# Kernel optimization log

Hardware: AMD Instinct MI355X
Metric: run time of the kernel (lower is better)

## Reference

```python
import jax, jax.numpy as jnp
import numpy as np

EPS = 1e-6
K = 20                 # k-NN neighbors (init default)
NEG_SLOPE_CONV = 0.2   # VNLinearLeakyReLU negative_slope in conv_pos / actvn_c
NEG_SLOPE_BLOCK = 0.0  # VNResnetBlockFC uses VNLeakyReLU(negative_slope=0.0)


def vn_linear(w, x):
    # w: [O, C], x: [B, C, 3, ...] -> [B, O, 3, ...]
    return jnp.einsum('oc,bc...->bo...', w, x)


def vn_leaky(x, d, slope):
    # Vector-neuron leaky ReLU: project onto learned direction d per channel.
    dot = jnp.sum(x * d, axis=2, keepdims=True)          # sum over 3-vector dim
    dsq = jnp.sum(d * d, axis=2, keepdims=True)
    x_neg = x - (dot / (dsq + EPS)) * d
    return slope * x + (1.0 - slope) * jnp.where(dot >= 0, x, x_neg)


def vn_lin_leaky(wf, wd, x, slope):
    return vn_leaky(vn_linear(wf, x), vn_linear(wd, x), slope)


def knn_idx(pts, k):
    # pts: [B, N, 3]; largest of negative squared distance = nearest (incl. self)
    d2 = jnp.sum(pts * pts, axis=-1)
    score = 2.0 * jnp.einsum('bnd,bmd->bnm', pts, pts) - d2[:, :, None] - d2[:, None, :]
    _, idx = jax.lax.top_k(score, k)
    return idx                                           # [B, N, k]


def graph_feature_cross(p, k):
    # p: [B, N, 3] -> edge features [B, 3(ch: rel, center, cross), 3(vec), N, k]
    idx = knn_idx(p, k)
    nb = jax.vmap(lambda pts, ix: pts[ix])(p, idx)       # [B, N, k, 3] gather
    ctr = jnp.broadcast_to(p[:, :, None, :], nb.shape)
    cross = jnp.cross(nb, ctr)
    feat = jnp.stack([nb - ctr, ctr, cross], axis=3)     # [B, N, k, 3ch, 3vec]
    return jnp.transpose(feat, (0, 3, 4, 1, 2))


def vn_resnet_block(x, wd0, wf0, wd1, wf1, wsc):
    net = vn_linear(wf0, vn_leaky(x, vn_linear(wd0, x), NEG_SLOPE_BLOCK))
    dx = vn_linear(wf1, vn_leaky(net, vn_linear(wd1, net), NEG_SLOPE_BLOCK))
    return vn_linear(wsc, x) + dx


def setup_inputs() -> dict:
    key = jax.random.key(0)
    ks = jax.random.split(key, 11)
    B, N = 4, 2048
    c_dim, hd = 128, 128
    s = lambda k_, sh, fan: (jax.random.normal(k_, sh, jnp.float32) / np.sqrt(fan).astype(np.float32))
    return {
        'p': jax.random.normal(ks[0], (B, N, 3), jnp.float32),
        'w_conv_feat': s(ks[1], (128, 3), 3),
        'w_conv_dir': s(ks[2], (128, 3), 3),
        'w_fc_pos': s(ks[3], (2 * hd, 128), 128),
        'blk_dir0': s(ks[4], (5, 2 * hd, 2 * hd), 2 * hd),
        'blk_fc0': s(ks[5], (5, hd, 2 * hd), 2 * hd),
        'blk_dir1': s(ks[6], (5, hd, hd), hd),
        'blk_fc1': s(ks[7], (5, hd, hd), hd),
        'blk_sc': s(ks[8], (5, hd, 2 * hd), 2 * hd),
        'w_actc_dir': s(ks[9], (hd, hd), hd),
        'w_fc_c': s(ks[10], (c_dim, hd), hd),
    }


def reference(p, w_conv_feat, w_conv_dir, w_fc_pos, blk_dir0, blk_fc0,
              blk_dir1, blk_fc1, blk_sc, w_actc_dir, w_fc_c):
    feat = graph_feature_cross(p, K)                     # [B, 3, 3, N, K]
    net = vn_lin_leaky(w_conv_feat, w_conv_dir, feat, NEG_SLOPE_CONV)
    net = net.mean(axis=-1)                              # pool over k -> [B,128,3,N]
    net = vn_linear(w_fc_pos, net)                       # [B,256,3,N]
    net = vn_resnet_block(net, blk_dir0[0], blk_fc0[0], blk_dir1[0], blk_fc1[0], blk_sc[0])
    for i in range(1, 5):                                # fixed 5-block stack
        pooled = jnp.broadcast_to(net.mean(axis=-1, keepdims=True), net.shape)
        net = jnp.concatenate([net, pooled], axis=1)     # [B,256,3,N]
        net = vn_resnet_block(net, blk_dir0[i], blk_fc0[i], blk_dir1[i], blk_fc1[i], blk_sc[i])
    net = net.mean(axis=-1)                              # global pool -> [B,128,3]
    net = vn_leaky(net, vn_linear(w_actc_dir, net), NEG_SLOPE_CONV)
    return vn_linear(w_fc_c, net)                        # c: [B,128,3]
```

## Files before the change

### kernel.cpp

```cpp
#include <hip/hip_runtime.h>
#include <math.h>

#define NPT 2048
#define BB 4
#define KNN 20
#define EPSV 1e-6f

typedef unsigned short u16;
typedef unsigned int u32;
typedef _Float16 half8 __attribute__((ext_vector_type(8)));
typedef __attribute__((ext_vector_type(4))) float f32x4;
typedef __attribute__((ext_vector_type(4))) u32 uint4v;

#define MFMAH(a,b,c) __builtin_amdgcn_mfma_f32_16x16x32_f16((a),(b),(c),0,0,0)

__device__ __forceinline__ u16 f2h(float f) {
    _Float16 h = (_Float16)f;
    return __builtin_bit_cast(u16, h);
}
__device__ __forceinline__ float h2f(u16 b) {
    return (float)__builtin_bit_cast(_Float16, b);
}

__global__ __launch_bounds__(256)
void knn_edge_kernel(const float* __restrict__ p,
                     const float* __restrict__ wf, const float* __restrict__ wd,
                     u16* __restrict__ net1) {
    int bn = blockIdx.x;
    int b = bn >> 11, n = bn & (NPT - 1);
    const float* pb = p + (size_t)b * NPT * 3;
    float qx = pb[n*3+0], qy = pb[n*3+1], qz = pb[n*3+2];
    float qq = qx*qx + qy*qy + qz*qz;
    __shared__ u32 keys[NPT];
    __shared__ int hist[4][256];
    __shared__ int wtot[4];
    __shared__ int sh_byte, sh_ngt, sure_cnt, tie_cnt;
    __shared__ int tie_m[64];
    __shared__ int sel[KNN];
    __shared__ float nb[KNN][3];
    int tid = threadIdx.x;
    int lane = tid & 63, wv = tid >> 6;
    for (int m = tid; m < NPT; m += 256) {
        float px = pb[m*3+0], py = pb[m*3+1], pz = pb[m*3+2];
        float sc = 2.f*(qx*px + qy*py + qz*pz) - qq - (px*px + py*py + pz*pz);
        u32 u = __builtin_bit_cast(u32, sc);
        keys[m] = u ^ (u32)(((int)u >> 31) | (int)0x80000000);
    }
    if (tid == 0) { sure_cnt = 0; tie_cnt = 0; }
    __syncthreads();
    u32 prefix = 0; int need = KNN;
    for (int pass = 3; pass >= 0; --pass) {
        int shift = pass * 8;
        u32 maskhi = (pass == 3) ? 0u : (0xFFFFFFFFu << (shift + 8));
        hist[0][tid] = 0; hist[1][tid] = 0; hist[2][tid] = 0; hist[3][tid] = 0;
        __syncthreads();
        int prevbin = -1, cnt = 0;
        #pragma unroll
        for (int j = 0; j < 8; ++j) {
            u32 key = keys[tid + 256*j];
            int bin = ((key & maskhi) == (prefix & maskhi)) ? (int)((key >> shift) & 255) : -1;
            if (bin == prevbin) { ++cnt; }
            else {
                if (prevbin >= 0) atomicAdd(&hist[wv][prevbin], cnt);
                prevbin = bin; cnt = 1;
            }
        }
        if (prevbin >= 0) atomicAdd(&hist[wv][prevbin], cnt);
        __syncthreads();
        int own = hist[0][tid] + hist[1][tid] + hist[2][tid] + hist[3][tid];
        int sum = own;
        #pragma unroll
        for (int off = 1; off < 64; off <<= 1) {
            int v = __shfl_down(sum, off, 64);
            if (lane + off < 64) sum += v;
        }
        if (lane == 0) wtot[wv] = sum;
        __syncthreads();
        int addhi = 0;
        #pragma unroll
        for (int w2 = 0; w2 < 4; ++w2) if (w2 > wv) addhi += wtot[w2];
        int cnt_ge = sum + addhi;
        int cnt_gt = cnt_ge - own;
        if (cnt_ge >= need && cnt_gt < need) { sh_byte = tid; sh_ngt = cnt_gt; }
        __syncthreads();
        prefix |= ((u32)sh_byte) << shift;
        need -= sh_ngt;
        __syncthreads();
    }
    u32 T = prefix;
    #pragma unroll
    for (int j = 0; j < 8; ++j) {
        int m = tid + 256*j;
        u32 key = keys[m];
        if (key > T) {
            int slot = atomicAdd(&sure_cnt, 1);
            sel[slot] = m;
        } else if (key == T) {
            int t = atomicAdd(&tie_cnt, 1);
            if (t < 64) tie_m[t] = m;
        }
    }
    __syncthreads();
    if (tid == 0) {
        int base = sure_cnt;
        int r = KNN - base;
        int tc = tie_cnt;
        if (tc == r) {
            for (int t2 = 0; t2 < r; ++t2) sel[base + t2] = tie_m[t2];
        } else if (tc <= 64) {
            for (int t2 = 0; t2 < r; ++t2) {
                int best = 1 << 30, bj = 0;
                for (int t3 = 0; t3 < tc; ++t3)
                    if (tie_m[t3] < best) { best = tie_m[t3]; bj = t3; }
                tie_m[bj] = 1 << 30;
                sel[base + t2] = best;
            }
        } else {
            int got = 0;
            for (int m = 0; m < NPT && got < r; ++m)
                if (keys[m] == T) { sel[base + got] = m; ++got; }
        }
    }
    __syncthreads();
    if (tid < KNN) {
        int j = sel[tid];
        nb[tid][0] = pb[j*3+0]; nb[tid][1] = pb[j*3+1]; nb[tid][2] = pb[j*3+2];
    }
    __syncthreads();
    {
        float* part = (float*)keys;
        int o = tid & 127, kh = tid >> 7;
        float wfa = wf[o*3+0], wfb = wf[o*3+1], wfc = wf[o*3+2];
        float wda = wd[o*3+0], wdb = wd[o*3+1], wdc = wd[o*3+2];
        float cx = qx, cy = qy, cz = qz;
        float a0 = 0.f, a1 = 0.f, a2 = 0.f;
        int k0 = kh * 10;
        #pragma unroll
        for (int k = 0; k < 10; ++k) {
            float nx = nb[k0+k][0], ny = nb[k0+k][1], nz = nb[k0+k][2];
            float rx = nx-cx, ry = ny-cy, rz = nz-cz;
            float sx = ny*cz - nz*cy;
            float sy = nz*cx - nx*cz;
            float sz = nx*cy - ny*cx;
            float fx = wfa*rx + wfb*cx + wfc*sx;
            float fy = wfa*ry + wfb*cy + wfc*sy;
            float fz = wfa*rz + wfb*cz + wfc*sz;
            float dx0 = wda*rx + wdb*cx + wdc*sx;
            float dy0 = wda*ry + wdb*cy + wdc*sy;
            float dz0 = wda*rz + wdb*cz + wdc*sz;
            float dot = fx*dx0 + fy*dy0 + fz*dz0;
            float dsq = dx0*dx0 + dy0*dy0 + dz0*dz0;
            float t = dot / (dsq + EPSV);
            bool pos = dot >= 0.f;
            float gx = pos ? fx : (fx - t*dx0);
            float gy = pos ? fy : (fy - t*dy0);
            float gz = pos ? fz : (fz - t*dz0);
            a0 += 0.2f*fx + 0.8f*gx;
            a1 += 0.2f*fy + 0.8f*gy;
            a2 += 0.2f*fz + 0.8f*gz;
        }
        if (kh == 1) { part[o*3+0] = a0; part[o*3+1] = a1; part[o*3+2] = a2; }
        __syncthreads();
        if (kh == 0) {
            a0 += part[o*3+0]; a1 += part[o*3+1]; a2 += part[o*3+2];
            const float s = 1.f / (float)KNN;
            net1[(size_t)(b*6144 +          n)*128 + o] = f2h(a0*s);
            net1[(size_t)(b*6144 + 2048  + n)*128 + o] = f2h(a1*s);
            net1[(size_t)(b*6144 + 4096  + n)*128 + o] = f2h(a2*s);
        }
    }
}

template<int O, int C1, int C2, bool POOL, bool BIASED>
__global__ __launch_bounds__(256) void gemm_plain(
    const u16* __restrict__ W1, int ldw1,
    const u16* __restrict__ X1, int sx1,
    const u16* __restrict__ W2, int ldw2,
    const u16* __restrict__ X2, int sx2,
    const float* __restrict__ WscF, const float* __restrict__ PmPrev,
    u16* __restrict__ Y, int sy,
    float* __restrict__ PmOut)
{
    __shared__ __align__(16) char smem[64*132*4];
    __shared__ float pms[128];
    __shared__ float biasS_s[128];
    const int m0 = blockIdx.x * 64;
    const int ob = blockIdx.y * 128;
    const int b   = m0 / 6144;
    const int vec = (m0 % 6144) / 2048;
    const int tid = threadIdx.x;
    const int lane = tid & 63;
    const int wid = __builtin_amdgcn_readfirstlane(tid >> 6);
    const int wr = wid & 1, wc = wid >> 1;
    const int l15 = lane & 15, l4 = lane >> 4;

    if (BIASED) {
        if (tid < 128) pms[tid] = PmPrev[(size_t)(b*128 + tid)*3 + vec];
        __syncthreads();
        if (tid < 128) {
            const float* wrow = WscF + (size_t)tid*256 + 128;
            float s = 0.f;
            #pragma unroll 4
            for (int c = 0; c < 128; ++c) s += wrow[c]*pms[c];
            biasS_s[tid] = s;
        }
        __syncthreads();
    }

    f32x4 acc[4][2];
    #pragma unroll
    for (int io = 0; io < 4; ++io) {
        float bv[4];
        #pragma unroll
        for (int r = 0; r < 4; ++r)
            bv[r] = BIASED ? biasS_s[wr*64 + io*16 + l4*4 + r] : 0.f;
        #pragma unroll
        for (int jc = 0; jc < 2; ++jc)
            #pragma unroll
            for (int r = 0; r < 4; ++r) acc[io][jc][r] = bv[r];
    }

    constexpr int NS = (C1 + C2) / 64;
    auto ldaddr = [&](int st, int u) -> const u16* {
        const bool ph2 = (st >= C1/64);
        const u16* w = ph2 ? W2 : W1; const u16* x = ph2 ? X2 : X1;
        int ldw = ph2 ? ldw2 : ldw1; int sx = ph2 ? sx2 : sx1;
        int cc = (ph2 ? (st - C1/64) : st) * 64;
        if (u < 1024) {
            int row = u >> 3, q = u & 7;
            return w + (size_t)(ob + row)*ldw + cc + q*8;
        }
        int uu = u - 1024;
        int row = uu >> 3, q = uu & 7;
        return x + (size_t)(m0 + row)*sx + cc + q*8;
    };
    auto lds_dst = [&](int u) -> char* {
        if (u < 1024) { int row = u >> 3, q = u & 7; return smem + row*144 + q*16; }
        int uu = u - 1024;
        int row = uu >> 3, q = uu & 7;
        return smem + 18432 + row*144 + q*16;
    };

    uint4v pf[6];
    #pragma unroll
    for (int j = 0; j < 6; ++j) pf[j] = *reinterpret_cast<const uint4v*>(ldaddr(0, tid + 256*j));
    #pragma unroll
    for (int j = 0; j < 6; ++j) *reinterpret_cast<uint4v*>(lds_dst(tid + 256*j)) = pf[j];

    for (int st = 0; st < NS; ++st) {
        __syncthreads();
        if (st + 1 < NS) {
            #pragma unroll
            for (int j = 0; j < 6; ++j)
                pf[j] = *reinterpret_cast<const uint4v*>(ldaddr(st+1, tid + 256*j));
        }
        #pragma unroll
        for (int ks = 0; ks < 2; ++ks) {
            half8 fA[4], fB[2];
            #pragma unroll
            for (int io = 0; io < 4; ++io)
                fA[io] = *reinterpret_cast<const half8*>(smem + (wr*64 + io*16 + l15)*144 + ks*64 + l4*16);
            #pragma unroll
            for (int i = 0; i < 2; ++i)
                fB[i] = *reinterpret_cast<const half8*>(smem + 18432 + (wc*32 + i*16 + l15)*144 + ks*64 + l4*16);
            #pragma unroll
            for (int io = 0; io < 4; ++io)
                #pragma unroll
                for (int jc = 0; jc < 2; ++jc)
                    acc[io][jc] = MFMAH(fA[io], fB[jc], acc[io][jc]);
        }
        __syncthreads();
        if (st + 1 < NS) {
            #pragma unroll
            for (int j = 0; j < 6; ++j)
                *reinterpret_cast<uint4v*>(lds_dst(tid + 256*j)) = pf[j];
        }
    }

    float* sd = (float*)smem;
    #pragma unroll
    for (int io = 0; io < 4; ++io)
        #pragma unroll
        for (int jc = 0; jc < 2; ++jc) {
            int jj = wc*32 + jc*16 + l15;
            int orow = wr*64 + io*16 + l4*4;
            *reinterpret_cast<f32x4*>(sd + jj*132 + orow) = acc[io][jc];
        }
    __syncthreads();

    #pragma unroll
    for (int rep = 0; rep < 4; ++rep) {
        int task = tid + 256*rep;
        int oc = task & 15, ml = task >> 4;
        const float* dp = sd + ml*132 + oc*8;
        u32 hw[4];
        #pragma unroll
        for (int e2 = 0; e2 < 4; ++e2)
            hw[e2] = (u32)f2h(dp[2*e2]) | ((u32)f2h(dp[2*e2+1]) << 16);
        *reinterpret_cast<uint4v*>(Y + (size_t)(m0 + ml)*sy + ob + oc*8) =
            (uint4v){hw[0],hw[1],hw[2],hw[3]};
    }

    if (POOL) {
        int o_l = tid & 127, half = tid >> 7;
        float sum = 0.f;
        #pragma unroll 8
        for (int c = 0; c < 32; ++c) sum += sd[(half*32 + c)*132 + o_l];
        atomicAdd(&PmOut[(size_t)(b*128 + o_l)*3 + vec], sum * (1.f/(float)NPT));
    }
}

template<int O, int CIN, bool VIRT>
__global__ __launch_bounds__(256) void gemm_dir(
    const u16* __restrict__ W_, int ldw,
    const u16* __restrict__ X1, int sx,
    const float* __restrict__ WdF, const float* __restrict__ Pm,
    u16* __restrict__ Ov, int so,
    float* __restrict__ PmZero)
{
    __shared__ __align__(16) char smem[96*132*4];
    __shared__ float pmd[384];
    __shared__ float biasD_s[384];
    const int gx = blockIdx.x;
    const int b  = gx >> 6;
    const int n0 = (gx & 63) * 32;
    const int ob = blockIdx.y * 128;
    const int tid = threadIdx.x;
    const int lane = tid & 63;
    const int wid = __builtin_amdgcn_readfirstlane(tid >> 6);
    const int wr = wid & 1, wc = wid >> 1;
    const int l15 = lane & 15, l4 = lane >> 4;

    if (PmZero != nullptr && gx == 0 && blockIdx.y == 0)
        for (int t = tid; t < 1536; t += 256) PmZero[t] = 0.f;

    if (VIRT) {
        for (int t = tid; t < 384; t += 256) pmd[t] = Pm[(size_t)b*384 + t];
        __syncthreads();
        for (int t = tid; t < 384; t += 256) {
            int o_l = t / 3, v = t - o_l*3;
            const float* wrow = WdF + (size_t)(ob + o_l)*256 + 128;
            float s = 0.f;
            #pragma unroll 4
            for (int c = 0; c < 128; ++c) s += wrow[c]*pmd[c*3 + v];
            biasD_s[t] = s;
        }
        __syncthreads();
    }

    f32x4 acc[4][3];
    #pragma unroll
    for (int io = 0; io < 4; ++io)
        #pragma unroll
        for (int jc = 0; jc < 3; ++jc) {
            int v = (wc*48 + jc*16) >> 5;
            #pragma unroll
            for (int r = 0; r < 4; ++r) {
                int o_l = wr*64 + io*16 + l4*4 + r;
                acc[io][jc][r] = VIRT ? biasD_s[o_l*3 + v] : 0.f;
            }
        }

    constexpr int NS = CIN / 64;
    auto ldaddr = [&](int st, int u) -> const u16* {
        int cc = st*64;
        if (u < 1024) {
            int row = u >> 3, q = u & 7;
            return W_ + (size_t)(ob + row)*ldw + cc + q*8;
        }
        int uu = u - 1024;
        int row = uu >> 3, q = uu & 7;
        int m = b*6144 + (row >> 5)*2048 + n0 + (row & 31);
        return X1 + (size_t)m*sx + cc + q*8;
    };
    auto lds_dst = [&](int u) -> char* {
        if (u < 1024) { int row = u >> 3, q = u & 7; return smem + row*144 + q*16; }
        int uu = u - 1024;
        int row = uu >> 3, q = uu & 7;
        return smem + 18432 + row*144 + q*16;
    };

    uint4v pf[7];
    #pragma unroll
    for (int j = 0; j < 7; ++j) pf[j] = *reinterpret_cast<const uint4v*>(ldaddr(0, tid + 256*j));
    #pragma unroll
    for (int j = 0; j < 7; ++j) *reinterpret_cast<uint4v*>(lds_dst(tid + 256*j)) = pf[j];

    for (int st = 0; st < NS; ++st) {
        __syncthreads();
        if (st + 1 < NS) {
            #pragma unroll
            for (int j = 0; j < 7; ++j)
                pf[j] = *reinterpret_cast<const uint4v*>(ldaddr(st+1, tid + 256*j));
        }
        #pragma unroll
        for (int ks = 0; ks < 2; ++ks) {
            half8 fA[4], fB[3];
            #pragma unroll
            for (int io = 0; io < 4; ++io)
                fA[io] = *reinterpret_cast<const half8*>(smem + (wr*64 + io*16 + l15)*144 + ks*64 + l4*16);
            #pragma unroll
            for (int i = 0; i < 3; ++i)
                fB[i] = *reinterpret_cast<const half8*>(smem + 18432 + (wc*48 + i*16 + l15)*144 + ks*64 + l4*16);
            #pragma unroll
            for (int io = 0; io < 4; ++io)
                #pragma unroll
                for (int jc = 0; jc < 3; ++jc)
                    acc[io][jc] = MFMAH(fA[io], fB[jc], acc[io][jc]);
        }
        __syncthreads();
        if (st + 1 < NS) {
            #pragma unroll
            for (int j = 0; j < 7; ++j)
                *reinterpret_cast<uint4v*>(lds_dst(tid + 256*j)) = pf[j];
        }
    }

    float* sd = (float*)smem;
    #pragma unroll
    for (int io = 0; io < 4; ++io)
        #pragma unroll
        for (int jc = 0; jc < 3; ++jc) {
            int jj = wc*48 + jc*16 + l15;
            int orow = wr*64 + io*16 + l4*4;
            *reinterpret_cast<f32x4*>(sd + jj*132 + orow) = acc[io][jc];
        }
    __syncthreads();

    #pragma unroll
    for (int rep = 0; rep < 2; ++rep) {
        int task = tid + 256*rep;
        int oc = task & 15, nl = (task >> 4) & 31;
        float d[3][8], x[3][8];
        #pragma unroll
        for (int v = 0; v < 3; ++v) {
            const float* dp = sd + (v*32 + nl)*132 + oc*8;
            #pragma unroll
            for (int e = 0; e < 8; ++e) d[v][e] = dp[e];
        }
        if (VIRT && ob != 0) {
            #pragma unroll
            for (int e = 0; e < 8; ++e) {
                int c = oc*8 + e;
                #pragma unroll
                for (int v = 0; v < 3; ++v)
                    x[v][e] = Pm[(size_t)(b*128 + c)*3 + v];
            }
        } else {
            #pragma unroll
            for (int v = 0; v < 3; ++v) {
                size_t m = (size_t)(b*6144 + v*2048 + n0 + nl);
                uint4v hx = *reinterpret_cast<const uint4v*>(X1 + m*sx + ob + oc*8);
                #pragma unroll
                for (int w = 0; w < 4; ++w) {
                    x[v][2*w]   = h2f((u16)(hx[w] & 0xffffu));
                    x[v][2*w+1] = h2f((u16)(hx[w] >> 16));
                }
            }
        }
        #pragma unroll
        for (int e = 0; e < 8; ++e) {
            float d0 = d[0][e], d1 = d[1][e], d2 = d[2][e];
            float dot = x[0][e]*d0 + x[1][e]*d1 + x[2][e]*d2;
            float dsq = d0*d0 + d1*d1 + d2*d2;
            float t = dot / (dsq + EPSV);
            if (dot < 0.f) { x[0][e] -= t*d0; x[1][e] -= t*d1; x[2][e] -= t*d2; }
        }
        #pragma unroll
        for (int v = 0; v < 3; ++v) {
            u32 hw[4];
            #pragma unroll
            for (int e2 = 0; e2 < 4; ++e2)
                hw[e2] = (u32)f2h(x[v][2*e2]) | ((u32)f2h(x[v][2*e2+1]) << 16);
            *reinterpret_cast<uint4v*>(Ov + (size_t)(b*6144 + v*2048 + n0 + nl)*so + ob + oc*8) =
                (uint4v){hw[0],hw[1],hw[2],hw[3]};
        }
    }
}

#define WO_FCPOS 0
#define WO_DIR0  32768
#define WO_FC0   360448
#define WO_DIR1  524288
#define WO_FC1   606208
#define WO_SC    688128
#define WTOT     851968
__global__ __launch_bounds__(256)
void convert_w_kernel(const float* __restrict__ s0, const float* __restrict__ s1,
                      const float* __restrict__ s2, const float* __restrict__ s3,
                      const float* __restrict__ s4, const float* __restrict__ s5,
                      u16* __restrict__ Wf) {
    int t = blockIdx.x*256 + threadIdx.x;
    if (t >= WTOT) return;
    const float* src; int base;
    if      (t < WO_DIR0) { src = s0; base = WO_FCPOS; }
    else if (t < WO_FC0)  { src = s1; base = WO_DIR0; }
    else if (t < WO_DIR1) { src = s2; base = WO_FC0; }
    else if (t < WO_FC1)  { src = s3; base = WO_DIR1; }
    else if (t < WO_SC)   { src = s4; base = WO_FC1; }
    else                  { src = s5; base = WO_SC; }
    Wf[t] = f2h(src[t - base]);
}

__global__ __launch_bounds__(128)
void final_head_kernel(const float* __restrict__ q, const float* __restrict__ Wdir,
                       const float* __restrict__ Wfc, float* __restrict__ out) {
    int b = blockIdx.x; int o = threadIdx.x;
    __shared__ float qs[128][3];
    __shared__ float zs[128][3];
    qs[o][0] = q[((size_t)b*128 + o)*3 + 0];
    qs[o][1] = q[((size_t)b*128 + o)*3 + 1];
    qs[o][2] = q[((size_t)b*128 + o)*3 + 2];
    __syncthreads();
    float d0 = 0.f, d1 = 0.f, d2 = 0.f;
    for (int c = 0; c < 128; ++c) {
        float w = Wdir[o*128 + c];
        d0 += w*qs[c][0]; d1 += w*qs[c][1]; d2 += w*qs[c][2];
    }
    float x0 = qs[o][0], x1 = qs[o][1], x2 = qs[o][2];
    float dot = d0*x0 + d1*x1 + d2*x2;
    float dsq = d0*d0 + d1*d1 + d2*d2;
    float t = dot / (dsq + EPSV);
    bool pos = dot >= 0.f;
    float g0 = pos ? x0 : (x0 - t*d0);
    float g1 = pos ? x1 : (x1 - t*d1);
    float g2 = pos ? x2 : (x2 - t*d2);
    zs[o][0] = 0.2f*x0 + 0.8f*g0;
    zs[o][1] = 0.2f*x1 + 0.8f*g1;
    zs[o][2] = 0.2f*x2 + 0.8f*g2;
    __syncthreads();
    float c0 = 0.f, c1 = 0.f, c2 = 0.f;
    for (int c = 0; c < 128; ++c) {
        float w = Wfc[o*128 + c];
        c0 += w*zs[c][0]; c1 += w*zs[c][1]; c2 += w*zs[c][2];
    }
    out[((size_t)b*128 + o)*3 + 0] = c0;
    out[((size_t)b*128 + o)*3 + 1] = c1;
    out[((size_t)b*128 + o)*3 + 2] = c2;
}

extern "C" void kernel_launch(void* const* d_in, const int* in_sizes, int n_in,
                              void* d_out, int out_size, void* d_ws, size_t ws_size,
                              hipStream_t stream) {
    const float* p           = (const float*)d_in[0];
    const float* w_conv_feat = (const float*)d_in[1];
    const float* w_conv_dir  = (const float*)d_in[2];
    const float* w_fc_pos    = (const float*)d_in[3];
    const float* blk_dir0    = (const float*)d_in[4];
    const float* blk_fc0     = (const float*)d_in[5];
    const float* blk_dir1    = (const float*)d_in[6];
    const float* blk_fc1     = (const float*)d_in[7];
    const float* blk_sc      = (const float*)d_in[8];
    const float* w_actc_dir  = (const float*)d_in[9];
    const float* w_fc_c      = (const float*)d_in[10];
    float* out = (float*)d_out;

    char* wsb = (char*)d_ws;
    size_t cur = 0;
    auto carve = [&](size_t nbytes) -> char* {
        char* r = wsb + cur;
        cur += (nbytes + 255) & ~(size_t)255;
        return r;
    };
    const size_t MTOT = (size_t)BB*3*NPT;
    float* Pm0   = (float*)carve(1536*4);
    float* Pm1   = (float*)carve(1536*4);
    u16* Wf    = (u16*)carve((size_t)WTOT*2);
    u16* net1  = (u16*)carve(MTOT*128*2);
    u16* X0    = (u16*)carve(MTOT*256*2);
    u16* Ab    = (u16*)carve(MTOT*256*2);
    u16* Yb    = (u16*)carve(MTOT*128*2);
    float* PmBuf[2] = { Pm0, Pm1 };

    convert_w_kernel<<<(WTOT+255)/256, 256, 0, stream>>>(
        w_fc_pos, blk_dir0, blk_fc0, blk_dir1, blk_fc1, blk_sc, Wf);
    knn_edge_kernel<<<BB*NPT, 256, 0, stream>>>(p, w_conv_feat, w_conv_dir, net1);

    gemm_plain<256,128,0,false,false><<<dim3(384,2), 256, 0, stream>>>(
        Wf+WO_FCPOS, 128, net1, 128,
        nullptr, 0, nullptr, 0,
        nullptr, nullptr, X0, 256, nullptr);

    const u16* Yp = nullptr;
    for (int i = 0; i < 5; ++i) {
        size_t od0 = WO_DIR0 + (size_t)i*65536;
        size_t of0 = WO_FC0  + (size_t)i*32768;
        size_t od1 = WO_DIR1 + (size_t)i*16384;
        size_t of1 = WO_FC1  + (size_t)i*16384;
        size_t osc = WO_SC   + (size_t)i*32768;
        float* PmPrev = PmBuf[(i+1) & 1];
        float* PmCur  = PmBuf[i & 1];

        if (i == 0) {
            gemm_dir<256,256,false><<<dim3(BB*64,2), 256, 0, stream>>>(
                Wf+od0, 256, X0, 256, nullptr, nullptr, Ab, 256, PmCur);
        } else {
            gemm_dir<256,128,true><<<dim3(BB*64,2), 256, 0, stream>>>(
                Wf+od0, 256, Yp, 128,
                blk_dir0 + (size_t)i*65536, PmPrev, Ab, 256, PmCur);
        }
        gemm_plain<128,256,0,false,false><<<dim3(384,1), 256, 0, stream>>>(
            Wf+of0, 256, Ab, 256,
            nullptr, 0, nullptr, 0,
            nullptr, nullptr, net1, 128, nullptr);
        gemm_dir<128,128,false><<<dim3(BB*64,1), 256, 0, stream>>>(
            Wf+od1, 128, net1, 128, nullptr, nullptr, Ab, 128, nullptr);

        u16* outv = (i % 2 == 0) ? Yb : X0;
        if (i == 0) {
            gemm_plain<128,128,256,true,false><<<dim3(384,1), 256, 0, stream>>>(
                Wf+of1, 128, Ab, 128,
                Wf+osc, 256, X0, 256,
                nullptr, nullptr, outv, 128, PmCur);
        } else {
            gemm_plain<128,128,128,true,true><<<dim3(384,1), 256, 0, stream>>>(
                Wf+of1, 128, Ab, 128,
                Wf+osc, 256, Yp, 128,
                blk_sc + (size_t)i*32768, PmPrev, outv, 128, PmCur);
        }
        Yp = outv;
    }

    final_head_kernel<<<BB, 128, 0, stream>>>(PmBuf[0], w_actc_dir, w_fc_c, out);
}
```

Baseline: 326.9 us.

## Fuse second direction GEMM, VN leaky ReLU and output/shortcut GEMM per block

Replaces the separate gemm_dir (dir1) and gemm_plain (fc1 + shortcut) launches in each resnet block with one fused kernel. It computes the direction projection, applies the VN leaky ReLU in shared memory, then runs the fc1 and shortcut GEMMs on the staged activations. This removes a global round trip of the intermediate activation buffer and one launch per block, five blocks in all. In exchange each workgroup holds all 128 output channels for 32 points and uses large shared memory (about 80KB), which may limit occupancy. The grid also drops from 384 to 256 workgroups.

```diff
diff --git a/kernel.cpp b/kernel.cpp
--- a/kernel.cpp
+++ b/kernel.cpp
@@ -478,6 +478,256 @@
     }
 }
 
+template<int CSC, bool VIRT>
+__global__ __launch_bounds__(256) void fused_back(
+    const u16* __restrict__ Wd,
+    const u16* __restrict__ Wf1,
+    const u16* __restrict__ Wsc,
+    const float* __restrict__ WsF,
+    const u16* __restrict__ T_,
+    const u16* __restrict__ Xs,
+    const float* __restrict__ Pm,
+    u16* __restrict__ Y,
+    float* __restrict__ PmOut)
+{
+    __shared__ __align__(16) char smem[76800];
+    __shared__ float pms[384];
+    __shared__ float biasS_s[384];
+    constexpr int U_OFF = 0;
+    constexpr int W_OFF = 26112;
+    constexpr int X_OFF = 44544;
+    const int gx = blockIdx.x;
+    const int b  = gx >> 6;
+    const int n0 = (gx & 63) * 32;
+    const int tid = threadIdx.x;
+    const int lane = tid & 63;
+    const int wid = __builtin_amdgcn_readfirstlane(tid >> 6);
+    const int wr = wid & 1, wc = wid >> 1;
+    const int l15 = lane & 15, l4 = lane >> 4;
+
+    if (VIRT) {
+        for (int t = tid; t < 384; t += 256) pms[t] = Pm[(size_t)b*384 + t];
+        __syncthreads();
+        for (int t = tid; t < 384; t += 256) {
+            int o_l = t / 3, v = t - o_l*3;
+            const float* wrow = WsF + (size_t)o_l*256 + 128;
+            float s = 0.f;
+            #pragma unroll 4
+            for (int c = 0; c < 128; ++c) s += wrow[c]*pms[c*3 + v];
+            biasS_s[t] = s;
+        }
+        __syncthreads();
+    }
+
+    f32x4 acc1[4][3];
+    #pragma unroll
+    for (int io = 0; io < 4; ++io)
+        #pragma unroll
+        for (int jc = 0; jc < 3; ++jc)
+            acc1[io][jc] = (f32x4){0.f,0.f,0.f,0.f};
+
+    auto ld1 = [&](int st, int u) -> const u16* {
+        int cc = st*64;
+        if (u < 1024) { int row = u >> 3, q = u & 7; return Wd + (size_t)row*128 + cc + q*8; }
+        int uu = u - 1024;
+        int row = uu >> 3, q = uu & 7;
+        int m = b*6144 + (row >> 5)*2048 + n0 + (row & 31);
+        return T_ + (size_t)m*128 + cc + q*8;
+    };
+    auto st1 = [&](int u) -> char* {
+        if (u < 1024) { int row = u >> 3, q = u & 7; return smem + W_OFF + row*144 + q*16; }
+        int uu = u - 1024;
+        int row = uu >> 3, q = uu & 7;
+        return smem + X_OFF + row*144 + q*16;
+    };
+
+    uint4v pf[7];
+    #pragma unroll
+    for (int j = 0; j < 7; ++j) pf[j] = *reinterpret_cast<const uint4v*>(ld1(0, tid + 256*j));
+    #pragma unroll
+    for (int j = 0; j < 7; ++j) *reinterpret_cast<uint4v*>(st1(tid + 256*j)) = pf[j];
+
+    for (int st = 0; st < 2; ++st) {
+        __syncthreads();
+        if (st + 1 < 2) {
+            #pragma unroll
+            for (int j = 0; j < 7; ++j)
+                pf[j] = *reinterpret_cast<const uint4v*>(ld1(st+1, tid + 256*j));
+        }
+        #pragma unroll
+        for (int ks = 0; ks < 2; ++ks) {
+            half8 fA[4], fB[3];
+            #pragma unroll
+            for (int io = 0; io < 4; ++io)
+                fA[io] = *reinterpret_cast<const half8*>(smem + W_OFF + (wr*64 + io*16 + l15)*144 + ks*64 + l4*16);
+            #pragma unroll
+            for (int i = 0; i < 3; ++i)
+                fB[i] = *reinterpret_cast<const half8*>(smem + X_OFF + (wc*48 + i*16 + l15)*144 + ks*64 + l4*16);
+            #pragma unroll
+            for (int io = 0; io < 4; ++io)
+                #pragma unroll
+                for (int jc = 0; jc < 3; ++jc)
+                    acc1[io][jc] = MFMAH(fA[io], fB[jc], acc1[io][jc]);
+        }
+        __syncthreads();
+        if (st + 1 < 2) {
+            #pragma unroll
+            for (int j = 0; j < 7; ++j)
+                *reinterpret_cast<uint4v*>(st1(tid + 256*j)) = pf[j];
+        }
+    }
+
+    float* sd = (float*)(smem + W_OFF);
+    #pragma unroll
+    for (int io = 0; io < 4; ++io)
+        #pragma unroll
+        for (int jc = 0; jc < 3; ++jc) {
+            int jj = wc*48 + jc*16 + l15;
+            int orow = wr*64 + io*16 + l4*4;
+            *reinterpret_cast<f32x4*>(sd + jj*132 + orow) = acc1[io][jc];
+        }
+    __syncthreads();
+    #pragma unroll
+    for (int rep = 0; rep < 2; ++rep) {
+        int task = tid + 256*rep;
+        int oc = task & 15, nl = (task >> 4) & 31;
+        float d[3][8], x[3][8];
+        #pragma unroll
+        for (int v = 0; v < 3; ++v) {
+            const float* dp = sd + (v*32 + nl)*132 + oc*8;
+            #pragma unroll
+            for (int e = 0; e < 8; ++e) d[v][e] = dp[e];
+        }
+        #pragma unroll
+        for (int v = 0; v < 3; ++v) {
+            size_t m = (size_t)(b*6144 + v*2048 + n0 + nl);
+            uint4v hx = *reinterpret_cast<const uint4v*>(T_ + m*128 + oc*8);
+            #pragma unroll
+            for (int w = 0; w < 4; ++w) {
+                x[v][2*w]   = h2f((u16)(hx[w] & 0xffffu));
+                x[v][2*w+1] = h2f((u16)(hx[w] >> 16));
+            }
+        }
+        #pragma unroll
+        for (int e = 0; e < 8; ++e) {
+            float d0 = d[0][e], d1 = d[1][e], d2 = d[2][e];
+            float dot = x[0][e]*d0 + x[1][e]*d1 + x[2][e]*d2;
+            float dsq = d0*d0 + d1*d1 + d2*d2;
+            float t = dot / (dsq + EPSV);
+            if (dot < 0.f) { x[0][e] -= t*d0; x[1][e] -= t*d1; x[2][e] -= t*d2; }
+        }
+        #pragma unroll
+        for (int v = 0; v < 3; ++v) {
+            u32 hw[4];
+            #pragma unroll
+            for (int e2 = 0; e2 < 4; ++e2)
+                hw[e2] = (u32)f2h(x[v][2*e2]) | ((u32)f2h(x[v][2*e2+1]) << 16);
+            *reinterpret_cast<uint4v*>(smem + U_OFF + (v*32 + nl)*272 + oc*16) =
+                (uint4v){hw[0],hw[1],hw[2],hw[3]};
+        }
+    }
+    __syncthreads();
+
+    f32x4 acc2[4][3];
+    #pragma unroll
+    for (int io = 0; io < 4; ++io)
+        #pragma unroll
+        for (int jc = 0; jc < 3; ++jc) {
+            int v = (wc*48 + jc*16) >> 5;
+            #pragma unroll
+            for (int r = 0; r < 4; ++r) {
+                int o_l = wr*64 + io*16 + l4*4 + r;
+                acc2[io][jc][r] = VIRT ? biasS_s[o_l*3 + v] : 0.f;
+            }
+        }
+
+    constexpr int NS2 = 2 + CSC/64;
+    auto ld2 = [&](int st, int u) -> const u16* {
+        if (st < 2) {
+            int row = u >> 3, q = u & 7;
+            return Wf1 + (size_t)row*128 + st*64 + q*8;
+        }
+        int cc = (st - 2)*64;
+        if (u < 1024) { int row = u >> 3, q = u & 7; return Wsc + (size_t)row*256 + cc + q*8; }
+        int uu = u - 1024;
+        int row = uu >> 3, q = uu & 7;
+        int m = b*6144 + (row >> 5)*2048 + n0 + (row & 31);
+        return Xs + (size_t)m*CSC + cc + q*8;
+    };
+
+    #pragma unroll
+    for (int j = 0; j < 7; ++j) { int u = tid + 256*j; if (u < 1024) pf[j] = *reinterpret_cast<const uint4v*>(ld2(0, u)); }
+    #pragma unroll
+    for (int j = 0; j < 7; ++j) { int u = tid + 256*j; if (u < 1024) *reinterpret_cast<uint4v*>(st1(u)) = pf[j]; }
+
+    for (int st = 0; st < NS2; ++st) {
+        __syncthreads();
+        int nv = (st + 1 < 2) ? 1024 : 1792;
+        if (st + 1 < NS2) {
+            #pragma unroll
+            for (int j = 0; j < 7; ++j) { int u = tid + 256*j; if (u < nv) pf[j] = *reinterpret_cast<const uint4v*>(ld2(st+1, u)); }
+        }
+        #pragma unroll
+        for (int ks = 0; ks < 2; ++ks) {
+            half8 fA[4], fB[3];
+            #pragma unroll
+            for (int io = 0; io < 4; ++io)
+                fA[io] = *reinterpret_cast<const half8*>(smem + W_OFF + (wr*64 + io*16 + l15)*144 + ks*64 + l4*16);
+            if (st < 2) {
+                #pragma unroll
+                for (int i = 0; i < 3; ++i)
+                    fB[i] = *reinterpret_cast<const half8*>(smem + U_OFF + (wc*48 + i*16 + l15)*272 + st*128 + ks*64 + l4*16);
+            } else {
+                #pragma unroll
+                for (int i = 0; i < 3; ++i)
+                    fB[i] = *reinterpret_cast<const half8*>(smem + X_OFF + (wc*48 + i*16 + l15)*144 + ks*64 + l4*16);
+            }
+            #pragma unroll
+            for (int io = 0; io < 4; ++io)
+                #pragma unroll
+                for (int jc = 0; jc < 3; ++jc)
+                    acc2[io][jc] = MFMAH(fA[io], fB[jc], acc2[io][jc]);
+        }
+        __syncthreads();
+        if (st + 1 < NS2) {
+            #pragma unroll
+            for (int j = 0; j < 7; ++j) { int u = tid + 256*j; if (u < nv) *reinterpret_cast<uint4v*>(st1(u)) = pf[j]; }
+        }
+    }
+
+    #pragma unroll
+    for (int io = 0; io < 4; ++io)
+        #pragma unroll
+        for (int jc = 0; jc < 3; ++jc) {
+            int jj = wc*48 + jc*16 + l15;
+            int orow = wr*64 + io*16 + l4*4;
+            *reinterpret_cast<f32x4*>(sd + jj*132 + orow) = acc2[io][jc];
+        }
+    __syncthreads();
+    #pragma unroll
+    for (int rep = 0; rep < 2; ++rep) {
+        int task = tid + 256*rep;
+        int oc = task & 15, nl = (task >> 4) & 31;
+        #pragma unroll
+        for (int v = 0; v < 3; ++v) {
+            const float* dp = sd + (v*32 + nl)*132 + oc*8;
+            u32 hw[4];
+            #pragma unroll
+            for (int e2 = 0; e2 < 4; ++e2)
+                hw[e2] = (u32)f2h(dp[2*e2]) | ((u32)f2h(dp[2*e2+1]) << 16);
+            *reinterpret_cast<uint4v*>(Y + (size_t)(b*6144 + v*2048 + n0 + nl)*128 + oc*8) =
+                (uint4v){hw[0],hw[1],hw[2],hw[3]};
+        }
+    }
+    for (int t = tid; t < 384; t += 256) {
+        int v = t >> 7, o_l = t & 127;
+        float sum = 0.f;
+        #pragma unroll 8
+        for (int nl = 0; nl < 32; ++nl) sum += sd[(v*32 + nl)*132 + o_l];
+        atomicAdd(&PmOut[(size_t)(b*128 + o_l)*3 + v], sum * (1.f/(float)NPT));
+    }
+}
+
 #define WO_FCPOS 0
 #define WO_DIR0  32768
 #define WO_FC0   360448
@@ -603,20 +853,16 @@
             Wf+of0, 256, Ab, 256,
             nullptr, 0, nullptr, 0,
             nullptr, nullptr, net1, 128, nullptr);
-        gemm_dir<128,128,false><<<dim3(BB*64,1), 256, 0, stream>>>(
-            Wf+od1, 128, net1, 128, nullptr, nullptr, Ab, 128, nullptr);
 
         u16* outv = (i % 2 == 0) ? Yb : X0;
         if (i == 0) {
-            gemm_plain<128,128,256,true,false><<<dim3(384,1), 256, 0, stream>>>(
-                Wf+of1, 128, Ab, 128,
-                Wf+osc, 256, X0, 256,
-                nullptr, nullptr, outv, 128, PmCur);
+            fused_back<256,false><<<BB*64, 256, 0, stream>>>(
+                Wf+od1, Wf+of1, Wf+osc, nullptr,
+                net1, X0, nullptr, outv, PmCur);
         } else {
-            gemm_plain<128,128,128,true,true><<<dim3(384,1), 256, 0, stream>>>(
-                Wf+of1, 128, Ab, 128,
-                Wf+osc, 256, Yp, 128,
-                blk_sc + (size_t)i*32768, PmPrev, outv, 128, PmCur);
+            fused_back<128,true><<<BB*64, 256, 0, stream>>>(
+                Wf+od1, Wf+of1, Wf+osc, blk_sc + (size_t)i*32768,
+                net1, Yp, PmPrev, outv, PmCur);
         }
         Yp = outv;
     }
```

Result: faster. 316.1 us (-3.3%).
